# Kernel tuning notes

Measured on AMD Instinct MI355X. Metric: run time of the kernel, lower is better.

## Reference

```python
import jax, jax.numpy as jnp
import numpy as np

COMMITMENT_COST = 0.25
N_TOKENS = 32768
NUM_EMBEDDINGS = 8192
EMBEDDING_DIM = 256


def setup_inputs() -> dict:
    key = jax.random.key(0)
    k1, k2 = jax.random.split(key)
    z_e = jax.random.normal(k1, (N_TOKENS, EMBEDDING_DIM), dtype=jnp.float32)
    embeddings = jax.random.normal(k2, (NUM_EMBEDDINGS, EMBEDDING_DIM), dtype=jnp.float32)
    return {"z_e": z_e, "embeddings": embeddings}


def reference(z_e, embeddings):
    # Pairwise squared L2 distances: ||z||^2 - 2 z.e + ||e||^2  -> (N, K)
    z_sq = jnp.sum(z_e * z_e, axis=-1, keepdims=True)          # (N, 1)
    e_sq = jnp.sum(embeddings * embeddings, axis=-1)            # (K,)
    cross = jnp.einsum('nd,kd->nk', z_e, embeddings)            # (N, K) GEMM
    distances = z_sq - 2.0 * cross + e_sq[None, :]
    encoding_indices = jnp.argmin(distances, axis=1)            # (N,)
    z_q = embeddings[encoding_indices]                          # gather (N, D)

    sg = jax.lax.stop_gradient
    commitment_loss = jnp.mean((sg(z_e) - z_q) ** 2)
    embedding_loss = jnp.mean((z_e - sg(z_q)) ** 2)
    vq_loss = embedding_loss + COMMITMENT_COST * commitment_loss

    # straight-through estimator
    z_q_st = z_e + sg(z_q - z_e)
    return z_q_st, vq_loss, encoding_indices
```

## Files before the change

kernel.cpp:

```cpp
#include <hip/hip_runtime.h>

typedef float f32x4 __attribute__((ext_vector_type(4)));
typedef short s16x8 __attribute__((ext_vector_type(8)));

#define NT 32768
#define NK 8192
#define ND 256
#define NSP 32
#define NKT 12

static __device__ __forceinline__ ushort f2bf(float f) {
  unsigned u = __float_as_uint(f);
  unsigned r = (u + 0x7FFFu + ((u >> 16) & 1u)) >> 16;
  return (ushort)r;
}

__global__ __launch_bounds__(256) void vq_cvt(const float* __restrict__ src,
                                              ushort* __restrict__ dst) {
  size_t idx = (size_t)blockIdx.x * 256 + threadIdx.x;
  size_t n = idx >> 6;
  int dq = (int)(idx & 63) * 4;
  float4 v = *reinterpret_cast<const float4*>(src + n * ND + dq);
  float f[4] = {v.x, v.y, v.z, v.w};
  ushort h[4], l[4];
#pragma unroll
  for (int t = 0; t < 4; ++t) {
    h[t] = f2bf(f[t]);
    float hf = __uint_as_float((unsigned)h[t] << 16);
    l[t] = f2bf(f[t] - hf);
  }
  *reinterpret_cast<ushort4*>(dst + n * 512 + dq) = make_ushort4(h[0], h[1], h[2], h[3]);
  *reinterpret_cast<ushort4*>(dst + n * 512 + 256 + dq) = make_ushort4(l[0], l[1], l[2], l[3]);
}

__global__ __launch_bounds__(256) void vq_esq(const float* __restrict__ emb,
                                              float* __restrict__ esq) {
  int w = threadIdx.x >> 6, lane = threadIdx.x & 63;
  int k = blockIdx.x * 4 + w;
  const float4 e = *reinterpret_cast<const float4*>(emb + (size_t)k * ND + lane * 4);
  float s = e.x * e.x + e.y * e.y + e.z * e.z + e.w * e.w;
#pragma unroll
  for (int off = 32; off >= 1; off >>= 1) s += __shfl_down(s, off);
  if (lane == 0) esq[k] = s;
}

#define GL16(gp, lp)                                                              \
  __builtin_amdgcn_global_load_lds(                                               \
      (const __attribute__((address_space(1))) unsigned int*)(gp),                \
      (__attribute__((address_space(3))) unsigned int*)(lp), 16, 0, 0)

#define BAR()                                                                     \
  do {                                                                            \
    asm volatile("" ::: "memory");                                                \
    __builtin_amdgcn_s_barrier();                                                 \
    asm volatile("" ::: "memory");                                                \
  } while (0)

__device__ __forceinline__ int koffA(int kt) { return ((kt >= 8) ? 256 : 0) + (kt & 3) * 64; }
__device__ __forceinline__ int koffB(int kt) { return ((kt >= 4 && kt < 8) ? 256 : 0) + (kt & 3) * 64; }

__global__ __launch_bounds__(512, 2) void vq_mfma(
    const ushort* __restrict__ z2, const ushort* __restrict__ e2,
    const float* __restrict__ esq, float* __restrict__ pdist,
    int* __restrict__ pidx) {
  __shared__ __align__(16) char smem[131072];
  char* ldsA = smem;
  char* ldsB = smem + 65536;

  const int gid = blockIdx.x;
  const int x = gid & 7, c = gid >> 3;
  const int S = x * 8 + (c >> 6);
  const int wi = c & 63;
  const int mt = (S >> 2) * 8 + (wi >> 3);
  const int nt = (S & 3) * 8 + (wi & 7);
  const int m0 = mt * 256, n0 = nt * 256;

  const int tid = threadIdx.x, lane = tid & 63, wid = tid >> 6;
  const int wr = wid >> 2, wc = wid & 3;
  const int fr = lane & 15, g = lane >> 4;

  const int sslot = (tid & 3) ^ ((tid >> 3) & 3);
  const ushort* aBase = z2 + (size_t)(m0 + (tid >> 2)) * 512 + sslot * 8;
  const ushort* bBase = e2 + (size_t)(n0 + (tid >> 2)) * 512 + sslot * 8;

#define STAGE_A(kt, kh)                                                           \
  do {                                                                            \
    const ushort* _g = aBase + koffA(kt) + (kh) * 32;                             \
    char* _l = ldsA + (((kt) & 1) << 15) + ((kh) << 14) + tid * 16;               \
    GL16(_g, _l);                                                                 \
    GL16(_g + 65536, _l + 8192);                                                  \
  } while (0)
#define STAGE_B(kt, kh)                                                           \
  do {                                                                            \
    const ushort* _g = bBase + koffB(kt) + (kh) * 32;                             \
    char* _l = ldsB + (((kt) & 1) << 15) + ((kh) << 14) + tid * 16;               \
    GL16(_g, _l);                                                                 \
    GL16(_g + 65536, _l + 8192);                                                  \
  } while (0)

  const int lbyte = fr * 64 + (((g ^ (fr >> 1)) & 3) << 4);
  const int aro = wr * 8192 + lbyte;
  const int bro = wc * 4096 + lbyte;

  f32x4 acc[8][4];
  const f32x4 zero = {0.f, 0.f, 0.f, 0.f};
#pragma unroll
  for (int i = 0; i < 8; ++i)
#pragma unroll
    for (int j = 0; j < 4; ++j) acc[i][j] = zero;

  STAGE_A(0, 0); STAGE_B(0, 0); STAGE_A(0, 1); STAGE_B(0, 1);
  asm volatile("s_waitcnt vmcnt(0)" ::: "memory");
  BAR();

#pragma unroll 2
  for (int kt = 0; kt < NKT; ++kt) {
    const int bufo = (kt & 1) << 15;
    const char* pa = ldsA + bufo + aro;
    const char* pb = ldsB + bufo + bro;

    if (kt + 1 < NKT) {
      STAGE_A(kt + 1, 0); STAGE_B(kt + 1, 0);
      STAGE_A(kt + 1, 1); STAGE_B(kt + 1, 1);
    }

    s16x8 af[8], bf[4];
#pragma unroll
    for (int j = 0; j < 4; ++j) bf[j] = *(const s16x8*)(pb + j * 1024);
#pragma unroll
    for (int i = 0; i < 8; ++i) af[i] = *(const s16x8*)(pa + i * 1024);
#pragma unroll
    for (int i = 0; i < 8; ++i)
#pragma unroll
      for (int j = 0; j < 4; ++j)
        acc[i][j] = __builtin_amdgcn_mfma_f32_16x16x32_bf16(af[i], bf[j], acc[i][j], 0, 0, 0);
#pragma unroll
    for (int j = 0; j < 4; ++j) bf[j] = *(const s16x8*)(pb + 16384 + j * 1024);
#pragma unroll
    for (int i = 0; i < 8; ++i) af[i] = *(const s16x8*)(pa + 16384 + i * 1024);
#pragma unroll
    for (int i = 0; i < 8; ++i)
#pragma unroll
      for (int j = 0; j < 4; ++j)
        acc[i][j] = __builtin_amdgcn_mfma_f32_16x16x32_bf16(af[i], bf[j], acc[i][j], 0, 0, 0);

    asm volatile("s_waitcnt vmcnt(0) lgkmcnt(0)" ::: "memory");
    __builtin_amdgcn_sched_barrier(0);
    BAR();
  }

  float eqv[4];
#pragma unroll
  for (int j = 0; j < 4; ++j) eqv[j] = esq[n0 + wc * 64 + j * 16 + fr];

  float* rdv = (float*)smem;
  unsigned char* rdc = (unsigned char*)(smem + 98304);

#pragma unroll
  for (int i = 0; i < 8; ++i)
#pragma unroll
    for (int r = 0; r < 4; ++r) {
      float bv = 3.4e38f; int bc = 0;
#pragma unroll
      for (int j = 0; j < 4; ++j) {
        float dist = fmaf(-2.f, acc[i][j][r], eqv[j]);
        int cl = wc * 64 + j * 16 + fr;
        if (dist < bv) { bv = dist; bc = cl; }
      }
      int row = wr * 128 + i * 16 + g * 4 + r;
      rdv[row * 67 + wc * 16 + fr] = bv;
      rdc[row * 64 + wc * 16 + fr] = (unsigned char)bc;
    }
  BAR();
  {
    const int row = tid >> 1, h = tid & 1;
    const float* pv = rdv + row * 67 + h * 32;
    const unsigned char* pc = rdc + row * 64 + h * 32;
    float bv = 3.4e38f; int bc = 256;
#pragma unroll
    for (int s = 0; s < 32; ++s) {
      float v = pv[s]; int cc = pc[s];
      if (v < bv || (v == bv && cc < bc)) { bv = v; bc = cc; }
    }
    float ov = __shfl_xor(bv, 1);
    int oc = __shfl_xor(bc, 1);
    if (ov < bv || (ov == bv && oc < bc)) { bv = ov; bc = oc; }
    if (h == 0) {
      int n = m0 + row;
      pdist[(size_t)n * NSP + nt] = bv;
      pidx[(size_t)n * NSP + nt] = n0 + bc;
    }
  }
}

__global__ __launch_bounds__(256) void vq_gather(
    const float* __restrict__ z, const float* __restrict__ emb,
    const float* __restrict__ pdist, const int* __restrict__ pidx,
    float* __restrict__ out, float* __restrict__ lpart) {
  int w = threadIdx.x >> 6, lane = threadIdx.x & 63;
  int n = blockIdx.x * 4 + w;
  int p = lane & (NSP - 1);
  float d = pdist[(size_t)n * NSP + p];
  int ii = pidx[(size_t)n * NSP + p];
#pragma unroll
  for (int off = 1; off < NSP; off <<= 1) {
    float od = __shfl_xor(d, off);
    int oi = __shfl_xor(ii, off);
    if (od < d || (od == d && oi < ii)) { d = od; ii = oi; }
  }
  int bi = ii;
  float4 q = *reinterpret_cast<const float4*>(emb + (size_t)bi * ND + lane * 4);
  float4 zz = *reinterpret_cast<const float4*>(z + (size_t)n * ND + lane * 4);
  *reinterpret_cast<float4*>(out + (size_t)n * ND + lane * 4) = q;
  float dx = zz.x - q.x, dy = zz.y - q.y, dz = zz.z - q.z, dw = zz.w - q.w;
  float s2 = dx * dx + dy * dy + dz * dz + dw * dw;
#pragma unroll
  for (int off = 32; off >= 1; off >>= 1) s2 += __shfl_down(s2, off);
  __shared__ float ls[4];
  if (lane == 0) {
    ls[w] = s2;
    out[(size_t)NT * ND + 1 + n] = (float)bi;
  }
  __syncthreads();
  if (threadIdx.x == 0) lpart[blockIdx.x] = ls[0] + ls[1] + ls[2] + ls[3];
}

__global__ __launch_bounds__(256) void vq_finalize(const float* __restrict__ lpart,
                                                   float* __restrict__ out) {
  __shared__ float s[256];
  float acc = 0.f;
  for (int i = threadIdx.x; i < NT / 4; i += 256) acc += lpart[i];
  s[threadIdx.x] = acc;
  __syncthreads();
  for (int st = 128; st >= 1; st >>= 1) {
    if (threadIdx.x < st) s[threadIdx.x] += s[threadIdx.x + st];
    __syncthreads();
  }
  if (threadIdx.x == 0)
    out[(size_t)NT * ND] = 1.25f * s[0] / (float)((size_t)NT * ND);
}

extern "C" void kernel_launch(void* const* d_in, const int* in_sizes, int n_in,
                              void* d_out, int out_size, void* d_ws, size_t ws_size,
                              hipStream_t stream) {
  const float* z = (const float*)d_in[0];
  const float* emb = (const float*)d_in[1];
  float* out = (float*)d_out;

  float* esq = (float*)d_ws;
  ushort* z2 = (ushort*)(esq + NK);
  ushort* e2 = z2 + (size_t)NT * 512;
  float* pdist = (float*)(e2 + (size_t)NK * 512);
  int* pidx = (int*)(pdist + (size_t)NT * NSP);
  float* lpart = (float*)(pidx + (size_t)NT * NSP);

  vq_cvt<<<NT / 4, 256, 0, stream>>>(z, z2);
  vq_cvt<<<NK / 4, 256, 0, stream>>>(emb, e2);
  vq_esq<<<NK / 4, 256, 0, stream>>>(emb, esq);
  vq_mfma<<<4096, 512, 0, stream>>>(z2, e2, esq, pdist, pidx);
  vq_gather<<<NT / 4, 256, 0, stream>>>(z, emb, pdist, pidx, out, lpart);
  vq_finalize<<<1, 256, 0, stream>>>(lpart, out);
}
```

Baseline: 447.7 us.

## Restructure GEMM main loop into ping-pong phases with staggered prefetch and setprio

Splits each K-tile iteration into four phases that each load a fragment slice from LDS, then issue 16 MFMAs bracketed by s_setprio. The global-to-LDS staging is split into halves issued one or two tiles ahead, with partial vmcnt waits in place of full drains. The goal is to overlap memory traffic with MFMA work and avoid the full vmcnt/lgkmcnt stall at the end of each iteration. In exchange it adds several extra barriers per iteration and a more fragile buffer-reuse schedule.

```diff
diff --git a/kernel.cpp b/kernel.cpp
--- a/kernel.cpp
+++ b/kernel.cpp
@@ -110,42 +110,87 @@
     for (int j = 0; j < 4; ++j) acc[i][j] = zero;
 
   STAGE_A(0, 0); STAGE_B(0, 0); STAGE_A(0, 1); STAGE_B(0, 1);
-  asm volatile("s_waitcnt vmcnt(0)" ::: "memory");
+  STAGE_B(1, 0); STAGE_A(1, 0);
+  asm volatile("s_waitcnt vmcnt(4)" ::: "memory");
   BAR();
+
+#define MFMA_PIN()                                                                \
+  do {                                                                            \
+    asm volatile("s_waitcnt lgkmcnt(0)" ::: "memory");                            \
+    __builtin_amdgcn_sched_barrier(0);                                            \
+    __builtin_amdgcn_s_setprio(1);                                                \
+  } while (0)
+#define MFMA_END()                                                                \
+  do {                                                                            \
+    __builtin_amdgcn_s_setprio(0);                                                \
+    __builtin_amdgcn_sched_barrier(0);                                            \
+  } while (0)
 
 #pragma unroll 2
   for (int kt = 0; kt < NKT; ++kt) {
     const int bufo = (kt & 1) << 15;
     const char* pa = ldsA + bufo + aro;
     const char* pb = ldsB + bufo + bro;
-
-    if (kt + 1 < NKT) {
-      STAGE_A(kt + 1, 0); STAGE_B(kt + 1, 0);
-      STAGE_A(kt + 1, 1); STAGE_B(kt + 1, 1);
+    s16x8 a0[4], a1[4], b[4];
+
+#pragma unroll
+    for (int j = 0; j < 4; ++j) b[j] = *(const s16x8*)(pb + j * 1024);
+#pragma unroll
+    for (int i = 0; i < 4; ++i) a0[i] = *(const s16x8*)(pa + i * 1024);
+    if (kt + 1 < NKT) { STAGE_B(kt + 1, 1); STAGE_A(kt + 1, 1); }
+    BAR();
+    MFMA_PIN();
+#pragma unroll
+    for (int i = 0; i < 4; ++i)
+#pragma unroll
+      for (int j = 0; j < 4; ++j)
+        acc[i][j] = __builtin_amdgcn_mfma_f32_16x16x32_bf16(a0[i], b[j], acc[i][j], 0, 0, 0);
+    MFMA_END();
+    BAR();
+
+#pragma unroll
+    for (int i = 0; i < 4; ++i) a1[i] = *(const s16x8*)(pa + (4 + i) * 1024);
+    if (kt + 2 < NKT) STAGE_B(kt + 2, 0);
+    BAR();
+    MFMA_PIN();
+#pragma unroll
+    for (int i = 0; i < 4; ++i)
+#pragma unroll
+      for (int j = 0; j < 4; ++j)
+        acc[4 + i][j] = __builtin_amdgcn_mfma_f32_16x16x32_bf16(a1[i], b[j], acc[4 + i][j], 0, 0, 0);
+    MFMA_END();
+    BAR();
+
+#pragma unroll
+    for (int j = 0; j < 4; ++j) b[j] = *(const s16x8*)(pb + 16384 + j * 1024);
+#pragma unroll
+    for (int i = 0; i < 4; ++i) a0[i] = *(const s16x8*)(pa + 16384 + i * 1024);
+    if (kt + 2 < NKT) STAGE_A(kt + 2, 0);
+    BAR();
+    MFMA_PIN();
+#pragma unroll
+    for (int i = 0; i < 4; ++i)
+#pragma unroll
+      for (int j = 0; j < 4; ++j)
+        acc[i][j] = __builtin_amdgcn_mfma_f32_16x16x32_bf16(a0[i], b[j], acc[i][j], 0, 0, 0);
+    MFMA_END();
+    BAR();
+
+#pragma unroll
+    for (int i = 0; i < 4; ++i) a1[i] = *(const s16x8*)(pa + 16384 + (4 + i) * 1024);
+    BAR();
+    MFMA_PIN();
+#pragma unroll
+    for (int i = 0; i < 4; ++i)
+#pragma unroll
+      for (int j = 0; j < 4; ++j)
+        acc[4 + i][j] = __builtin_amdgcn_mfma_f32_16x16x32_bf16(a1[i], b[j], acc[4 + i][j], 0, 0, 0);
+    MFMA_END();
+    if (kt < NKT - 2) {
+      asm volatile("s_waitcnt vmcnt(4)" ::: "memory");
+    } else {
+      asm volatile("s_waitcnt vmcnt(0)" ::: "memory");
     }
-
-    s16x8 af[8], bf[4];
-#pragma unroll
-    for (int j = 0; j < 4; ++j) bf[j] = *(const s16x8*)(pb + j * 1024);
-#pragma unroll
-    for (int i = 0; i < 8; ++i) af[i] = *(const s16x8*)(pa + i * 1024);
-#pragma unroll
-    for (int i = 0; i < 8; ++i)
-#pragma unroll
-      for (int j = 0; j < 4; ++j)
-        acc[i][j] = __builtin_amdgcn_mfma_f32_16x16x32_bf16(af[i], bf[j], acc[i][j], 0, 0, 0);
-#pragma unroll
-    for (int j = 0; j < 4; ++j) bf[j] = *(const s16x8*)(pb + 16384 + j * 1024);
-#pragma unroll
-    for (int i = 0; i < 8; ++i) af[i] = *(const s16x8*)(pa + 16384 + i * 1024);
-#pragma unroll
-    for (int i = 0; i < 8; ++i)
-#pragma unroll
-      for (int j = 0; j < 4; ++j)
-        acc[i][j] = __builtin_amdgcn_mfma_f32_16x16x32_bf16(af[i], bf[j], acc[i][j], 0, 0, 0);
-
-    asm volatile("s_waitcnt vmcnt(0) lgkmcnt(0)" ::: "memory");
-    __builtin_amdgcn_sched_barrier(0);
     BAR();
   }
 
```

New measurement: 455.7 us. Within noise of the previous version (+1.8%).

## Switch GEMM to 32x32x16 MFMA with 4 waves and interleaved prefetch

Applied to the files above, without the earlier changes.

Moves the distance GEMM from 16x16x32 bf16 MFMA with 8 waves per block to 32x32x16 MFMA with 4 waves, each wave owning a 128x128 tile. The global-to-LDS prefetch is now split into quarter stages issued between the k-substeps, with a partial vmcnt wait so loads overlap compute more deeply. The goal is fewer LDS reads per FLOP, since larger MFMA tiles reuse each fragment more, and better latency hiding. The price is fewer waves per CU, higher register pressure from 256 accumulator floats per thread, and extra barriers inside the k-loop.

```diff
diff --git a/kernel.cpp b/kernel.cpp
--- a/kernel.cpp
+++ b/kernel.cpp
@@ -1,6 +1,7 @@
 #include <hip/hip_runtime.h>
 
 typedef float f32x4 __attribute__((ext_vector_type(4)));
+typedef float f32x16 __attribute__((ext_vector_type(16)));
 typedef short s16x8 __attribute__((ext_vector_type(8)));
 
 #define NT 32768
@@ -59,7 +60,7 @@
 __device__ __forceinline__ int koffA(int kt) { return ((kt >= 8) ? 256 : 0) + (kt & 3) * 64; }
 __device__ __forceinline__ int koffB(int kt) { return ((kt >= 4 && kt < 8) ? 256 : 0) + (kt & 3) * 64; }
 
-__global__ __launch_bounds__(512, 2) void vq_mfma(
+__global__ __launch_bounds__(256, 1) void vq_mfma(
     const ushort* __restrict__ z2, const ushort* __restrict__ e2,
     const float* __restrict__ esq, float* __restrict__ pdist,
     int* __restrict__ pidx) {
@@ -76,8 +77,9 @@
   const int m0 = mt * 256, n0 = nt * 256;
 
   const int tid = threadIdx.x, lane = tid & 63, wid = tid >> 6;
-  const int wr = wid >> 2, wc = wid & 3;
-  const int fr = lane & 15, g = lane >> 4;
+  const int wr = wid >> 1, wc = wid & 1;
+  const int ll = lane & 31, h = lane >> 5;
+  const int pbase = (ll >> 1) & 3;
 
   const int sslot = (tid & 3) ^ ((tid >> 3) & 3);
   const ushort* aBase = z2 + (size_t)(m0 + (tid >> 2)) * 512 + sslot * 8;
@@ -87,109 +89,105 @@
   do {                                                                            \
     const ushort* _g = aBase + koffA(kt) + (kh) * 32;                             \
     char* _l = ldsA + (((kt) & 1) << 15) + ((kh) << 14) + tid * 16;               \
-    GL16(_g, _l);                                                                 \
-    GL16(_g + 65536, _l + 8192);                                                  \
+    GL16(_g, _l);                 GL16(_g + 32768, _l + 4096);                    \
+    GL16(_g + 65536, _l + 8192);  GL16(_g + 98304, _l + 12288);                   \
   } while (0)
 #define STAGE_B(kt, kh)                                                           \
   do {                                                                            \
     const ushort* _g = bBase + koffB(kt) + (kh) * 32;                             \
     char* _l = ldsB + (((kt) & 1) << 15) + ((kh) << 14) + tid * 16;               \
-    GL16(_g, _l);                                                                 \
-    GL16(_g + 65536, _l + 8192);                                                  \
+    GL16(_g, _l);                 GL16(_g + 32768, _l + 4096);                    \
+    GL16(_g + 65536, _l + 8192);  GL16(_g + 98304, _l + 12288);                   \
   } while (0)
 
-  const int lbyte = fr * 64 + (((g ^ (fr >> 1)) & 3) << 4);
-  const int aro = wr * 8192 + lbyte;
-  const int bro = wc * 4096 + lbyte;
-
-  f32x4 acc[8][4];
-  const f32x4 zero = {0.f, 0.f, 0.f, 0.f};
-#pragma unroll
-  for (int i = 0; i < 8; ++i)
-#pragma unroll
-    for (int j = 0; j < 4; ++j) acc[i][j] = zero;
+  const int arb = (wr * 128 + ll) * 64;
+  const int brb = (wc * 128 + ll) * 64;
+
+  f32x16 acc[4][4];
+#pragma unroll
+  for (int i = 0; i < 4; ++i)
+#pragma unroll
+    for (int j = 0; j < 4; ++j)
+#pragma unroll
+      for (int r = 0; r < 16; ++r) acc[i][j][r] = 0.f;
 
   STAGE_A(0, 0); STAGE_B(0, 0); STAGE_A(0, 1); STAGE_B(0, 1);
-  asm volatile("s_waitcnt vmcnt(0)" ::: "memory");
+  STAGE_A(1, 0); STAGE_B(1, 0);
+  asm volatile("s_waitcnt vmcnt(8)" ::: "memory");
   BAR();
 
 #pragma unroll 2
   for (int kt = 0; kt < NKT; ++kt) {
     const int bufo = (kt & 1) << 15;
-    const char* pa = ldsA + bufo + aro;
-    const char* pb = ldsB + bufo + bro;
-
-    if (kt + 1 < NKT) {
-      STAGE_A(kt + 1, 0); STAGE_B(kt + 1, 0);
-      STAGE_A(kt + 1, 1); STAGE_B(kt + 1, 1);
-    }
-
-    s16x8 af[8], bf[4];
-#pragma unroll
-    for (int j = 0; j < 4; ++j) bf[j] = *(const s16x8*)(pb + j * 1024);
-#pragma unroll
-    for (int i = 0; i < 8; ++i) af[i] = *(const s16x8*)(pa + i * 1024);
-#pragma unroll
-    for (int i = 0; i < 8; ++i)
-#pragma unroll
-      for (int j = 0; j < 4; ++j)
-        acc[i][j] = __builtin_amdgcn_mfma_f32_16x16x32_bf16(af[i], bf[j], acc[i][j], 0, 0, 0);
-#pragma unroll
-    for (int j = 0; j < 4; ++j) bf[j] = *(const s16x8*)(pb + 16384 + j * 1024);
-#pragma unroll
-    for (int i = 0; i < 8; ++i) af[i] = *(const s16x8*)(pa + 16384 + i * 1024);
-#pragma unroll
-    for (int i = 0; i < 8; ++i)
-#pragma unroll
-      for (int j = 0; j < 4; ++j)
-        acc[i][j] = __builtin_amdgcn_mfma_f32_16x16x32_bf16(af[i], bf[j], acc[i][j], 0, 0, 0);
-
-    asm volatile("s_waitcnt vmcnt(0) lgkmcnt(0)" ::: "memory");
-    __builtin_amdgcn_sched_barrier(0);
+    const char* pa = ldsA + bufo + arb;
+    const char* pb = ldsB + bufo + brb;
+    s16x8 a[4], b[4];
+
+#pragma unroll
+    for (int ks = 0; ks < 4; ++ks) {
+      const int ko = (ks >> 1) * 16384;
+      const int so = (((((ks & 1) << 1) | h) ^ pbase)) << 4;
+#pragma unroll
+      for (int mi = 0; mi < 4; ++mi) a[mi] = *(const s16x8*)(pa + ko + mi * 2048 + so);
+#pragma unroll
+      for (int ni = 0; ni < 4; ++ni) b[ni] = *(const s16x8*)(pb + ko + ni * 2048 + so);
+      BAR();
+      if (ks == 0)      { if (kt + 1 < NKT) STAGE_A(kt + 1, 1); }
+      else if (ks == 1) { if (kt + 1 < NKT) STAGE_B(kt + 1, 1); }
+      else if (ks == 2) { if (kt + 2 < NKT) STAGE_A(kt + 2, 0); }
+      else              { if (kt + 2 < NKT) STAGE_B(kt + 2, 0); }
+      asm volatile("s_waitcnt lgkmcnt(0)" ::: "memory");
+      __builtin_amdgcn_sched_barrier(0);
+#pragma unroll
+      for (int mi = 0; mi < 4; ++mi)
+#pragma unroll
+        for (int ni = 0; ni < 4; ++ni)
+          acc[mi][ni] = __builtin_amdgcn_mfma_f32_32x32x16_bf16(a[mi], b[ni], acc[mi][ni], 0, 0, 0);
+    }
+    if (kt < NKT - 2) {
+      asm volatile("s_waitcnt vmcnt(8)" ::: "memory");
+    } else {
+      asm volatile("s_waitcnt vmcnt(0)" ::: "memory");
+    }
     BAR();
   }
 
   float eqv[4];
 #pragma unroll
-  for (int j = 0; j < 4; ++j) eqv[j] = esq[n0 + wc * 64 + j * 16 + fr];
+  for (int ni = 0; ni < 4; ++ni) eqv[ni] = esq[n0 + wc * 128 + ni * 32 + ll];
 
   float* rdv = (float*)smem;
-  unsigned char* rdc = (unsigned char*)(smem + 98304);
-
-#pragma unroll
-  for (int i = 0; i < 8; ++i)
-#pragma unroll
-    for (int r = 0; r < 4; ++r) {
+  unsigned char* rdc = (unsigned char*)(smem + 69632);
+
+#pragma unroll
+  for (int mi = 0; mi < 4; ++mi)
+#pragma unroll
+    for (int reg = 0; reg < 16; ++reg) {
       float bv = 3.4e38f; int bc = 0;
 #pragma unroll
-      for (int j = 0; j < 4; ++j) {
-        float dist = fmaf(-2.f, acc[i][j][r], eqv[j]);
-        int cl = wc * 64 + j * 16 + fr;
+      for (int ni = 0; ni < 4; ++ni) {
+        float dist = fmaf(-2.f, acc[mi][ni][reg], eqv[ni]);
+        int cl = wc * 128 + ni * 32 + ll;
         if (dist < bv) { bv = dist; bc = cl; }
       }
-      int row = wr * 128 + i * 16 + g * 4 + r;
-      rdv[row * 67 + wc * 16 + fr] = bv;
-      rdc[row * 64 + wc * 16 + fr] = (unsigned char)bc;
+      int row = wr * 128 + mi * 32 + (reg & 3) + 8 * (reg >> 2) + 4 * h;
+      rdv[row * 68 + wc * 32 + ll] = bv;
+      rdc[row * 64 + wc * 32 + ll] = (unsigned char)bc;
     }
   BAR();
   {
-    const int row = tid >> 1, h = tid & 1;
-    const float* pv = rdv + row * 67 + h * 32;
-    const unsigned char* pc = rdc + row * 64 + h * 32;
+    const int row = tid;
+    const float* pv = rdv + row * 68;
+    const unsigned char* pc = rdc + row * 64;
     float bv = 3.4e38f; int bc = 256;
-#pragma unroll
-    for (int s = 0; s < 32; ++s) {
+#pragma unroll 8
+    for (int s = 0; s < 64; ++s) {
       float v = pv[s]; int cc = pc[s];
       if (v < bv || (v == bv && cc < bc)) { bv = v; bc = cc; }
     }
-    float ov = __shfl_xor(bv, 1);
-    int oc = __shfl_xor(bc, 1);
-    if (ov < bv || (ov == bv && oc < bc)) { bv = ov; bc = oc; }
-    if (h == 0) {
-      int n = m0 + row;
-      pdist[(size_t)n * NSP + nt] = bv;
-      pidx[(size_t)n * NSP + nt] = n0 + bc;
-    }
+    int n = m0 + row;
+    pdist[(size_t)n * NSP + nt] = bv;
+    pidx[(size_t)n * NSP + nt] = n0 + bc;
   }
 }
 
@@ -257,7 +255,7 @@
   vq_cvt<<<NT / 4, 256, 0, stream>>>(z, z2);
   vq_cvt<<<NK / 4, 256, 0, stream>>>(emb, e2);
   vq_esq<<<NK / 4, 256, 0, stream>>>(emb, esq);
-  vq_mfma<<<4096, 512, 0, stream>>>(z2, e2, esq, pdist, pidx);
+  vq_mfma<<<4096, 256, 0, stream>>>(z2, e2, esq, pdist, pidx);
   vq_gather<<<NT / 4, 256, 0, stream>>>(z, emb, pdist, pidx, out, lpart);
   vq_finalize<<<1, 256, 0, stream>>>(lpart, out);
 }
```

Result: slower. 595.0 us (+32.9%).
